# Kernel optimization log

Hardware: AMD Instinct MI355X
Metric: run time of the kernel (lower is better)

## Reference

```python
import jax, jax.numpy as jnp
import numpy as np

D = 1024   # input_size == hidden_size (tied weights)
H = 1024
V = 32000
STEPS = 5  # mogrify_steps
B = 32
T = 64


def _mogrify(x, h, W, b):
    # W: [STEPS, H, H] (square since D == H), b: [STEPS, H]
    for i in range(STEPS):
        if (i + 1) % 2 == 0:
            h = 2.0 * jax.nn.sigmoid(x @ W[i].T + b[i]) * h
        else:
            x = 2.0 * jax.nn.sigmoid(h @ W[i].T + b[i]) * x
    return x, h


def _lstm_cell(x, h, c, W_ih, W_hh, b_ih, b_hh):
    g = x @ W_ih.T + b_ih + h @ W_hh.T + b_hh  # [B, 4H], gate order i,f,g,o
    i, f, gg, o = jnp.split(g, 4, axis=-1)
    c = jax.nn.sigmoid(f) * c + jax.nn.sigmoid(i) * jnp.tanh(gg)
    h = jax.nn.sigmoid(o) * jnp.tanh(c)
    return h, c


def setup_inputs() -> dict:
    key = jax.random.key(0)
    ks = jax.random.split(key, 16)
    s = 1.0 / np.sqrt(H)
    u = lambda k, shape: jax.random.uniform(k, shape, jnp.float32, -s, s)
    return {
        "seq": jax.random.randint(ks[0], (B, T), 0, V),
        "max_len": T,
        "emb": jax.random.normal(ks[1], (V, D), jnp.float32) * 0.02,  # tied with fc weight
        "mog1_W": u(ks[2], (STEPS, H, H)), "mog1_b": u(ks[3], (STEPS, H)),
        "W_ih1": u(ks[4], (4 * H, D)), "W_hh1": u(ks[5], (4 * H, H)),
        "b_ih1": u(ks[6], (4 * H,)), "b_hh1": u(ks[7], (4 * H,)),
        "mog2_W": u(ks[8], (STEPS, H, H)), "mog2_b": u(ks[9], (STEPS, H)),
        "W_ih2": u(ks[10], (4 * H, H)), "W_hh2": u(ks[11], (4 * H, H)),
        "b_ih2": u(ks[12], (4 * H,)), "b_hh2": u(ks[13], (4 * H,)),
        "fc_b": u(ks[14], (V,)),
    }


def reference(seq, max_len, emb, mog1_W, mog1_b, W_ih1, W_hh1, b_ih1, b_hh1,
              mog2_W, mog2_b, W_ih2, W_hh2, b_ih2, b_hh2, fc_b):
    batch = seq.shape[0]
    embed = emb[seq[:, :max_len]]              # [B, T, D]
    xs = jnp.transpose(embed, (1, 0, 2))       # [T, B, D]
    h1 = jnp.zeros((batch, H), embed.dtype)
    c1 = jnp.zeros((batch, H), embed.dtype)
    h2 = jnp.zeros((batch, H), embed.dtype)
    c2 = jnp.zeros((batch, H), embed.dtype)

    def step(carry, x):
        h1, c1, h2, c2 = carry
        x1, h1m = _mogrify(x, h1, mog1_W, mog1_b)
        h1, c1 = _lstm_cell(x1, h1m, c1, W_ih1, W_hh1, b_ih1, b_hh1)
        x2, h2m = _mogrify(h1, h2, mog2_W, mog2_b)
        h2, c2 = _lstm_cell(x2, h2m, c2, W_ih2, W_hh2, b_ih2, b_hh2)
        return (h1, c1, h2, c2), h2

    _, hs = jax.lax.scan(step, (h1, c1, h2, c2), xs)   # hs: [T, B, H]
    hidden_states = jnp.transpose(hs, (1, 0, 2))        # [B, T, H]
    # fc weight tied to embedding -> logits = h @ emb.T + b (single big GEMM)
    outputs = jnp.einsum('bth,vh->btv', hidden_states, emb) + fc_b  # [B, T, V]
    return outputs, hidden_states
```

## Files before the change

### kernel.cpp

```cpp
#include <hip/hip_runtime.h>

typedef short bf16x8 __attribute__((ext_vector_type(8)));
typedef float f32x4 __attribute__((ext_vector_type(4)));
typedef unsigned int u32;
typedef u32 u32x4 __attribute__((ext_vector_type(4)));
typedef unsigned short u16;
typedef unsigned long long u64;

static __device__ __forceinline__ unsigned short f2bf(float f) {
    unsigned int u = __float_as_uint(f);
    unsigned int r = (u + 0x7fffu + ((u >> 16) & 1u)) >> 16;
    return (unsigned short)r;
}
static __device__ __forceinline__ float sigmoidf_(float x) {
    return 1.0f / (1.0f + __expf(-x));
}
static __device__ __forceinline__ float tanhf_(float x) {
    return 2.0f / (1.0f + __expf(-2.0f * x)) - 1.0f;
}

static __device__ __forceinline__ u32 pkhi(float a, float b) {
    return (__float_as_uint(a) >> 16) | (__float_as_uint(b) & 0xffff0000u);
}
static __device__ __forceinline__ u32 pklo(float a, float b) {
    float la = a - __uint_as_float(__float_as_uint(a) & 0xffff0000u);
    float lb = b - __uint_as_float(__float_as_uint(b) & 0xffff0000u);
    return (__float_as_uint(la) >> 16) | (__float_as_uint(lb) & 0xffff0000u);
}
static __device__ __forceinline__ bf16x8 mkfrag(u32 a, u32 b, u32 c, u32 d) {
    u32x4 v = {a, b, c, d};
    return __builtin_bit_cast(bf16x8, v);
}

static __device__ __forceinline__ bf16x8 ldA(const u16* p) {
    u64 a = __hip_atomic_load((const u64*)p, __ATOMIC_RELAXED, __HIP_MEMORY_SCOPE_AGENT);
    u64 b = __hip_atomic_load((const u64*)(p + 4), __ATOMIC_RELAXED, __HIP_MEMORY_SCOPE_AGENT);
    union { u64 q[2]; bf16x8 v; } u;
    u.q[0] = a; u.q[1] = b;
    return u.v;
}
static __device__ __forceinline__ float ldc4(const float* p) {
    return __hip_atomic_load(p, __ATOMIC_RELAXED, __HIP_MEMORY_SCOPE_AGENT);
}
static __device__ __forceinline__ void stc4(float* p, float v) {
    __hip_atomic_store(p, v, __ATOMIC_RELAXED, __HIP_MEMORY_SCOPE_AGENT);
}
static __device__ __forceinline__ void stc2(u16* p, u16 v) {
    __hip_atomic_store(p, v, __ATOMIC_RELAXED, __HIP_MEMORY_SCOPE_AGENT);
}

static __device__ __forceinline__ void dma16(const float* g, float* l) {
    __builtin_amdgcn_global_load_lds((const __attribute__((address_space(1))) void*)g,
                                     (__attribute__((address_space(3))) void*)l, 16, 0, 0);
}

static __device__ __forceinline__ void arrA(u32* bar, int line) {
    asm volatile("s_waitcnt vmcnt(0) lgkmcnt(0)" ::: "memory");
    __builtin_amdgcn_s_barrier();
    if (threadIdx.x == 0)
        __hip_atomic_fetch_add(bar + line * 32, 1u, __ATOMIC_RELAXED, __HIP_MEMORY_SCOPE_AGENT);
}
static __device__ __forceinline__ void arrP(u32* bar, int line) {
    __builtin_amdgcn_s_barrier();
    if (threadIdx.x == 0)
        __hip_atomic_fetch_add(bar + line * 32, 1u, __ATOMIC_RELAXED, __HIP_MEMORY_SCOPE_AGENT);
}
static __device__ __forceinline__ void bwait(u32* bar, int layer, bool master,
                                             bool glob, u32 target) {
    if (master) {
        if (threadIdx.x < 64) {
            const u32 tgt = glob ? (target << 8) : (target << 7);
            int line = glob ? (int)threadIdx.x : layer * 32 + (int)(threadIdx.x & 31);
            bool on = glob || (threadIdx.x < 32);
            for (;;) {
                u32 v = on ? __hip_atomic_load(bar + line * 32, __ATOMIC_RELAXED,
                                               __HIP_MEMORY_SCOPE_AGENT) : 0u;
                v += __shfl_xor(v, 1);
                v += __shfl_xor(v, 2);
                v += __shfl_xor(v, 4);
                v += __shfl_xor(v, 8);
                v += __shfl_xor(v, 16);
                v += __shfl_xor(v, 32);
                if (v >= tgt) break;
                __builtin_amdgcn_s_sleep(1);
            }
            if (threadIdx.x == 0)
                __hip_atomic_store(bar + 2112 + layer * 32, target, __ATOMIC_RELAXED,
                                   __HIP_MEMORY_SCOPE_AGENT);
        }
    } else {
        if (threadIdx.x == 0) {
            while (__hip_atomic_load(bar + 2112 + layer * 32, __ATOMIC_RELAXED,
                                     __HIP_MEMORY_SCOPE_AGENT) < target)
                __builtin_amdgcn_s_sleep(1);
        }
    }
    __builtin_amdgcn_s_barrier();
    asm volatile("" ::: "memory");
}

static __device__ __forceinline__ void stage_mogF(const float* W, int jb, float* lbuf,
                                                  int lane, int wv) {
    int oct2 = lane >> 5, row = (lane >> 1) & 15, half = lane & 1;
#pragma unroll
    for (int i = 0; i < 16; ++i) {
        int og = wv * 16 + i;
        const float* src = W + (size_t)(jb + row) * 1024 + (og * 2 + oct2) * 8 + half * 4;
        dma16(src, lbuf + og * 256);
    }
}
static __device__ __forceinline__ void stage_l128(const float* Ws, int jb, int kb,
                                                  float* lbuf, int lane, int wv) {
    int half = lane & 1;
#pragma unroll
    for (int i = 0; i < 8; ++i) {
        int octl = wv * 4 + (i >> 1);
        int rh = i & 1;
        int rowc = rh * 32 + (lane >> 1);
        int grow = (rowc >> 4) * 1024 + jb + (rowc & 15);
        const float* src = Ws + (size_t)grow * 1024 + kb + octl * 8 + half * 4;
        dma16(src, lbuf + octl * 512 + rh * 256);
    }
}

static __device__ __forceinline__ void l_acts(const u16* aH, const u16* aL, int cidx,
                                              int lane, int wv, bf16x8 fr[4]) {
    const int col = lane & 15, kq4 = lane >> 4;
    size_t octa = (size_t)cidx * 16 + wv * 4 + kq4;
    const u16* pH = aH + (octa * 32 + col) * 8;
    const u16* pL = aL + (octa * 32 + col) * 8;
    fr[0] = ldA(pH);
    fr[1] = ldA(pH + 128);
    fr[2] = ldA(pL);
    fr[3] = ldA(pL + 128);
}
static __device__ __forceinline__ void l_mfma(const float* lbuf, const bf16x8 fr[4],
                                              int lane, int wv, f32x4 (&acc)[4][2]) {
    const int col = lane & 15, kq4 = lane >> 4;
    const float* wbase = lbuf + (wv * 4 + kq4) * 512;
#pragma unroll
    for (int rt = 0; rt < 4; ++rt) {
        const float* wp = wbase + (rt * 16 + col) * 8;
        f32x4 w0 = *(const f32x4*)wp, w1 = *(const f32x4*)(wp + 4);
        bf16x8 whi = mkfrag(pkhi(w0.x, w0.y), pkhi(w0.z, w0.w),
                            pkhi(w1.x, w1.y), pkhi(w1.z, w1.w));
        bf16x8 wlo = mkfrag(pklo(w0.x, w0.y), pklo(w0.z, w0.w),
                            pklo(w1.x, w1.y), pklo(w1.z, w1.w));
        acc[rt][0] = __builtin_amdgcn_mfma_f32_16x16x32_bf16(fr[0], whi, acc[rt][0], 0, 0, 0);
        acc[rt][0] = __builtin_amdgcn_mfma_f32_16x16x32_bf16(fr[2], whi, acc[rt][0], 0, 0, 0);
        acc[rt][0] = __builtin_amdgcn_mfma_f32_16x16x32_bf16(fr[0], wlo, acc[rt][0], 0, 0, 0);
        acc[rt][1] = __builtin_amdgcn_mfma_f32_16x16x32_bf16(fr[1], whi, acc[rt][1], 0, 0, 0);
        acc[rt][1] = __builtin_amdgcn_mfma_f32_16x16x32_bf16(fr[3], whi, acc[rt][1], 0, 0, 0);
        acc[rt][1] = __builtin_amdgcn_mfma_f32_16x16x32_bf16(fr[1], wlo, acc[rt][1], 0, 0, 0);
    }
}

struct RArgs {
    const float *m1W, *m1b, *Wih1, *Whh1, *bih1, *bhh1;
    const float *m2W, *m2b, *Wih2, *Whh2, *bih2, *bhh2;
    float* XTF;
    u16 *XTH, *XTL;
    float* stF;
    u16* stH;
    float* hs;
    u32* bar;
};

__global__ __launch_bounds__(256, 1) void reck(RArgs A) {
    __shared__ float wbuf[4][8192];
    __shared__ float red[4][32][16];

    const int tid = threadIdx.x, lane = tid & 63, wv = tid >> 6;
    const int col = lane & 15, kq4 = lane >> 4;
    const int blk = blockIdx.x;
    const int layer = blk >> 7;
    const int g = blk & 127;
    const bool isMog = g < 64;
    const bool master = (g == 0);
    const int line = layer * 32 + (g & 31);
    const int jb = (g & 63) * 16;

    const float* mW  = layer ? A.m2W : A.m1W;
    const float* mb_ = layer ? A.m2b : A.m1b;
    const float* Wih = layer ? A.Wih2 : A.Wih1;
    const float* Whh = layer ? A.Whh2 : A.Whh1;
    const float* bih = layer ? A.bih2 : A.bih1;
    const float* bhh = layer ? A.bhh2 : A.bhh1;

    float* hF  = A.stF + layer * 32768;
    float* hmF = A.stF + 65536 + layer * 32768;
    float* cS  = A.stF + 131072 + layer * 32768;
    float* rFb = A.stF + 196608;
    u16* hH  = A.stH + layer * 32768;
    u16* hmH = A.stH + 65536 + layer * 32768;
    u16* rHb = A.stH + 131072;
    u16* hL  = A.stH + 196608 + layer * 32768;
    u16* hmL = A.stH + 262144 + layer * 32768;
    u16* rLb = A.stH + 327680;

    float* mbuf0 = &wbuf[0][0];
    float* mbuf1 = &wbuf[2][0];

    u32 bcnt = 0;
    int cur = 0;

    if (isMog) stage_mogF(mW, jb, mbuf0, lane, wv);

    for (int s = 0; s <= 64; ++s) {
        const bool act = layer ? (s > 0) : (s < 64);
        const int t = layer ? s - 1 : s;
        const int tt = act ? t : 0;
        const int rb = tt & 1;

        float* xF; u16 *xH, *xL;
        if (layer == 0) {
            xF = A.XTF + (size_t)tt * 32768;
            xH = A.XTH + (size_t)tt * 32768;
            xL = A.XTL + (size_t)tt * 32768;
        } else {
            xF = rFb + rb * 32768;
            xH = rHb + rb * 32768;
            xL = rLb + rb * 32768;
        }

        if (isMog) {
            for (int ph = 0; ph < 5; ++ph) {
                float* wsrc = cur ? mbuf1 : mbuf0;
                float* wdst = cur ? mbuf0 : mbuf1;
                if (act) {
                    const u16 *gH, *gL; const float* srcF; float* dF; u16 *dH, *dL;
                    switch (ph) {
                        case 0:  gH = hH;  gL = hL;  srcF = xF;  dF = xF;  dH = xH;  dL = xL;  break;
                        case 1:  gH = xH;  gL = xL;  srcF = hF;  dF = hmF; dH = hmH; dL = hmL; break;
                        case 2:  gH = hmH; gL = hmL; srcF = xF;  dF = xF;  dH = xH;  dL = xL;  break;
                        case 3:  gH = xH;  gL = xL;  srcF = hmF; dF = hmF; dH = hmH; dL = hmL; break;
                        default: gH = hmH; gL = hmL; srcF = xF;  dF = xF;  dH = xH;  dL = xL;  break;
                    }
                    bf16x8 AH0[8], AH1[8], AL0[8], AL1[8];
#pragma unroll
                    for (int kt = 0; kt < 8; ++kt) {
                        int octc = wv * 32 + kt * 4 + kq4;
                        const u16* pH = gH + ((size_t)octc * 32 + col) * 8;
                        const u16* pL = gL + ((size_t)octc * 32 + col) * 8;
                        AH0[kt] = ldA(pH);  AH1[kt] = ldA(pH + 128);
                        AL0[kt] = ldA(pL);  AL1[kt] = ldA(pL + 128);
                    }
                    stage_mogF(mW + (size_t)((ph + 1) % 5) * 1048576, jb, wdst, lane, wv);
                    f32x4 a0 = {0.f, 0.f, 0.f, 0.f}, a1 = {0.f, 0.f, 0.f, 0.f};
#pragma unroll
                    for (int kt = 0; kt < 8; ++kt) {
                        int octc = wv * 32 + kt * 4 + kq4;
                        const float* wp = wsrc + octc * 128 + col * 8;
                        f32x4 w0 = *(const f32x4*)wp, w1 = *(const f32x4*)(wp + 4);
                        bf16x8 whi = mkfrag(pkhi(w0.x, w0.y), pkhi(w0.z, w0.w),
                                            pkhi(w1.x, w1.y), pkhi(w1.z, w1.w));
                        bf16x8 wlo = mkfrag(pklo(w0.x, w0.y), pklo(w0.z, w0.w),
                                            pklo(w1.x, w1.y), pklo(w1.z, w1.w));
                        a0 = __builtin_amdgcn_mfma_f32_16x16x32_bf16(AH0[kt], whi, a0, 0, 0, 0);
                        a0 = __builtin_amdgcn_mfma_f32_16x16x32_bf16(AL0[kt], whi, a0, 0, 0, 0);
                        a0 = __builtin_amdgcn_mfma_f32_16x16x32_bf16(AH0[kt], wlo, a0, 0, 0, 0);
                        a1 = __builtin_amdgcn_mfma_f32_16x16x32_bf16(AH1[kt], whi, a1, 0, 0, 0);
                        a1 = __builtin_amdgcn_mfma_f32_16x16x32_bf16(AL1[kt], whi, a1, 0, 0, 0);
                        a1 = __builtin_amdgcn_mfma_f32_16x16x32_bf16(AH1[kt], wlo, a1, 0, 0, 0);
                    }
#pragma unroll
                    for (int mh = 0; mh < 2; ++mh) {
                        f32x4 av = mh ? a1 : a0;
#pragma unroll
                        for (int r = 0; r < 4; ++r)
                            red[wv][mh * 16 + kq4 * 4 + r][col] = av[r];
                    }
                    __syncthreads();
#pragma unroll
                    for (int uu = 0; uu < 2; ++uu) {
                        int u = tid + uu * 256;
                        int jj = u & 15, bb = u >> 4;
                        float sv = red[0][bb][jj] + red[1][bb][jj]
                                 + red[2][bb][jj] + red[3][bb][jj];
                        int d = jb + jj;
                        sv += mb_[ph * 1024 + d];
                        float gate = 2.0f * sigmoidf_(sv);
                        size_t pidx = ((size_t)(d >> 3) * 32 + bb) * 8 + (d & 7);
                        float val = gate * ldc4(srcF + pidx);
                        stc4(dF + pidx, val);
                        u32 uv = __float_as_uint(val);
                        stc2(dH + pidx, (u16)(uv >> 16));
                        float lov = val - __uint_as_float(uv & 0xffff0000u);
                        stc2(dL + pidx, (u16)(__float_as_uint(lov) >> 16));
                    }
                } else {
                    stage_mogF(mW + (size_t)((ph + 1) % 5) * 1048576, jb, wdst, lane, wv);
                }
                arrA(A.bar, line);
                ++bcnt;
                bwait(A.bar, layer, master, false, bcnt);
                cur ^= 1;
            }
            arrP(A.bar, line);
            ++bcnt;
            bwait(A.bar, layer, master, true, bcnt);
        } else {
            if (act) {
#pragma unroll
                for (int c = 0; c < 4; ++c)
                    stage_l128(Whh, jb, c * 128, &wbuf[c][0], lane, wv);
            }
#pragma unroll
            for (int p = 0; p < 4; ++p) {
                arrP(A.bar, line);
                ++bcnt;
                bwait(A.bar, layer, false, false, bcnt);
            }
            arrP(A.bar, line);
            ++bcnt;
            u32 g5t = bcnt;
            f32x4 acc[4][2];
#pragma unroll
            for (int rt = 0; rt < 4; ++rt) {
                acc[rt][0] = (f32x4){0.f, 0.f, 0.f, 0.f};
                acc[rt][1] = (f32x4){0.f, 0.f, 0.f, 0.f};
            }
            if (act) {
                for (int c = 0; c < 8; ++c) {
                    bf16x8 fr[4];
                    l_acts(hmH, hmL, c, lane, wv, fr);
                    l_mfma(&wbuf[c & 3][0], fr, lane, wv, acc);
                    int cn = c + 4;
                    if (cn < 8) stage_l128(Whh, jb, cn * 128, &wbuf[cn & 3][0], lane, wv);
                    else        stage_l128(Wih, jb, (cn - 8) * 128, &wbuf[cn & 3][0], lane, wv);
                }
            }
            bwait(A.bar, layer, false, false, g5t);
            if (act) {
                for (int c = 8; c < 16; ++c) {
                    bf16x8 fr[4];
                    l_acts(xH, xL, c - 8, lane, wv, fr);
                    l_mfma(&wbuf[c & 3][0], fr, lane, wv, acc);
                    int cn = c + 4;
                    if (cn < 16) stage_l128(Wih, jb, (cn - 8) * 128, &wbuf[cn & 3][0], lane, wv);
                }
                float gv[2][4];
#pragma unroll
                for (int gt = 0; gt < 4; ++gt) {
                    __syncthreads();
#pragma unroll
                    for (int mh = 0; mh < 2; ++mh) {
                        f32x4 av = acc[gt][mh];
#pragma unroll
                        for (int r = 0; r < 4; ++r)
                            red[wv][mh * 16 + kq4 * 4 + r][col] = av[r];
                    }
                    __syncthreads();
#pragma unroll
                    for (int uu = 0; uu < 2; ++uu) {
                        int u = tid + uu * 256;
                        gv[uu][gt] = red[0][u >> 4][u & 15] + red[1][u >> 4][u & 15]
                                   + red[2][u >> 4][u & 15] + red[3][u >> 4][u & 15];
                    }
                }
#pragma unroll
                for (int uu = 0; uu < 2; ++uu) {
                    int u = tid + uu * 256;
                    int cell = u & 15, bb = u >> 4;
                    int d = jb + cell;
                    float gi = gv[uu][0] + bih[d] + bhh[d];
                    float gf = gv[uu][1] + bih[1024 + d] + bhh[1024 + d];
                    float gg = gv[uu][2] + bih[2048 + d] + bhh[2048 + d];
                    float go = gv[uu][3] + bih[3072 + d] + bhh[3072 + d];
                    int cidx = d * 32 + bb;
                    float cn = sigmoidf_(gf) * cS[cidx] + sigmoidf_(gi) * tanhf_(gg);
                    cS[cidx] = cn;
                    float hn = sigmoidf_(go) * tanhf_(cn);
                    size_t pidx = ((size_t)(d >> 3) * 32 + bb) * 8 + (d & 7);
                    u32 uv = __float_as_uint(hn);
                    u16 hhi = (u16)(uv >> 16);
                    float lov = hn - __uint_as_float(uv & 0xffff0000u);
                    u16 hlo = (u16)(__float_as_uint(lov) >> 16);
                    stc4(hF + pidx, hn);
                    stc2(hH + pidx, hhi);
                    stc2(hL + pidx, hlo);
                    if (layer == 0) {
                        int wb = s & 1;
                        stc4(rFb + wb * 32768 + pidx, hn);
                        stc2(rHb + wb * 32768 + pidx, hhi);
                        stc2(rLb + wb * 32768 + pidx, hlo);
                    } else {
                        A.hs[(size_t)bb * 65536 + (size_t)t * 1024 + d] = hn;
                    }
                }
                arrA(A.bar, line);
            } else {
                arrP(A.bar, line);
            }
            ++bcnt;
            bwait(A.bar, layer, false, true, bcnt);
        }
    }
}

__global__ __launch_bounds__(256) void gather_embed(const int* __restrict__ seq,
                                                    const float* __restrict__ emb,
                                                    float* __restrict__ XTF,
                                                    u16* __restrict__ XTH,
                                                    u16* __restrict__ XTL) {
    int t = blockIdx.x;
#pragma unroll 4
    for (int i = 0; i < 16; ++i) {
        int u = i * 256 + threadIdx.x;
        int oct = u >> 5, b = u & 31;
        int row = seq[b * 64 + t];
        const float* sp = emb + (size_t)row * 1024 + oct * 8;
        float4 f0 = *(const float4*)sp;
        float4 f1 = *(const float4*)(sp + 4);
        size_t base = (size_t)t * 32768 + ((size_t)oct * 32 + b) * 8;
        *(float4*)(XTF + base) = f0;
        *(float4*)(XTF + base + 4) = f1;
        u32x4 hi = {pkhi(f0.x, f0.y), pkhi(f0.z, f0.w), pkhi(f1.x, f1.y), pkhi(f1.z, f1.w)};
        u32x4 lo = {pklo(f0.x, f0.y), pklo(f0.z, f0.w), pklo(f1.x, f1.y), pklo(f1.z, f1.w)};
        *(u32x4*)(XTH + base) = hi;
        *(u32x4*)(XTL + base) = lo;
    }
}

__global__ __launch_bounds__(256) void f32_to_bf16(const float* __restrict__ in,
                                                   unsigned short* __restrict__ out, int n) {
    int i = (blockIdx.x * 256 + threadIdx.x) * 8;
    if (i + 7 < n) {
        float4 f0 = *(const float4*)(in + i);
        float4 f1 = *(const float4*)(in + i + 4);
        bf16x8 v;
        v[0] = (short)f2bf(f0.x); v[1] = (short)f2bf(f0.y);
        v[2] = (short)f2bf(f0.z); v[3] = (short)f2bf(f0.w);
        v[4] = (short)f2bf(f1.x); v[5] = (short)f2bf(f1.y);
        v[6] = (short)f2bf(f1.z); v[7] = (short)f2bf(f1.w);
        *(bf16x8*)(out + i) = v;
    }
}

__global__ __launch_bounds__(256) void out_proj(const unsigned short* __restrict__ hsb,
                                                const float* __restrict__ emb,
                                                const float* __restrict__ fcb,
                                                float* __restrict__ out) {
    __shared__ unsigned short Al[128 * 40];
    __shared__ unsigned short Bl[128 * 40];
    int tid = threadIdx.x;
    int n0 = blockIdx.x * 128;
    int m0 = blockIdx.y * 128;
    int wid = tid >> 6, l = tid & 63;
    int wm = wid >> 1, wn = wid & 1;
    int c16 = l & 15, kg = l >> 4;

    f32x4 acc[4][4];
#pragma unroll
    for (int i = 0; i < 4; i++)
#pragma unroll
        for (int j = 0; j < 4; j++) acc[i][j] = (f32x4){0.f, 0.f, 0.f, 0.f};

    for (int k0 = 0; k0 < 1024; k0 += 32) {
#pragma unroll
        for (int i = 0; i < 2; i++) {
            int id = i * 256 + tid;
            int r = id >> 2, ccc = id & 3;
            *(bf16x8*)&Al[r * 40 + ccc * 8] =
                *(const bf16x8*)(hsb + (size_t)(m0 + r) * 1024 + k0 + ccc * 8);
        }
#pragma unroll
        for (int i = 0; i < 2; i++) {
            int id = i * 256 + tid;
            int r = id >> 2, ccc = id & 3;
            const float* src = emb + (size_t)(n0 + r) * 1024 + k0 + ccc * 8;
            float4 f0 = *(const float4*)(src);
            float4 f1 = *(const float4*)(src + 4);
            bf16x8 v;
            v[0] = (short)f2bf(f0.x); v[1] = (short)f2bf(f0.y);
            v[2] = (short)f2bf(f0.z); v[3] = (short)f2bf(f0.w);
            v[4] = (short)f2bf(f1.x); v[5] = (short)f2bf(f1.y);
            v[6] = (short)f2bf(f1.z); v[7] = (short)f2bf(f1.w);
            *(bf16x8*)&Bl[r * 40 + ccc * 8] = v;
        }
        __syncthreads();

        bf16x8 afr[4], bfr[4];
#pragma unroll
        for (int i = 0; i < 4; i++)
            afr[i] = *(const bf16x8*)&Al[(wm * 64 + i * 16 + c16) * 40 + kg * 8];
#pragma unroll
        for (int j = 0; j < 4; j++)
            bfr[j] = *(const bf16x8*)&Bl[(wn * 64 + j * 16 + c16) * 40 + kg * 8];
#pragma unroll
        for (int i = 0; i < 4; i++)
#pragma unroll
            for (int j = 0; j < 4; j++)
                acc[i][j] = __builtin_amdgcn_mfma_f32_16x16x32_bf16(afr[i], bfr[j], acc[i][j], 0, 0, 0);
        __syncthreads();
    }

#pragma unroll
    for (int i = 0; i < 4; i++) {
        int row = m0 + wm * 64 + i * 16 + kg * 4;
#pragma unroll
        for (int j = 0; j < 4; j++) {
            int col = n0 + wn * 64 + j * 16 + c16;
            float fb = fcb[col];
#pragma unroll
            for (int r = 0; r < 4; r++)
                out[(size_t)(row + r) * 32000 + col] = acc[i][j][r] + fb;
        }
    }
}

extern "C" void kernel_launch(void* const* d_in, const int* in_sizes, int n_in,
                              void* d_out, int out_size, void* d_ws, size_t ws_size,
                              hipStream_t stream) {
    const int*   seq    = (const int*)d_in[0];
    const float* emb    = (const float*)d_in[2];
    const float* mog1_W = (const float*)d_in[3];
    const float* mog1_b = (const float*)d_in[4];
    const float* W_ih1  = (const float*)d_in[5];
    const float* W_hh1  = (const float*)d_in[6];
    const float* b_ih1  = (const float*)d_in[7];
    const float* b_hh1  = (const float*)d_in[8];
    const float* mog2_W = (const float*)d_in[9];
    const float* mog2_b = (const float*)d_in[10];
    const float* W_ih2  = (const float*)d_in[11];
    const float* W_hh2  = (const float*)d_in[12];
    const float* b_ih2  = (const float*)d_in[13];
    const float* b_hh2  = (const float*)d_in[14];
    const float* fc_b   = (const float*)d_in[15];

    char* ws = (char*)d_ws;
    float* XTF = (float*)ws;
    u16*   XTH = (u16*)(ws + 8388608);
    u16*   XTL = (u16*)(ws + 12582912);
    float* stF = (float*)(ws + 16777216);
    u16*   stH = (u16*)(ws + 17825792);
    u32*   bar = (u32*)(ws + 18874368);
    unsigned short* hsb = (unsigned short*)(ws + 18890752);

    float* out0 = (float*)d_out;
    float* hs   = out0 + 65536000LL;

    hipMemsetAsync(stF, 0, 1835008, stream);
    hipMemsetAsync(bar, 0, 16384, stream);

    gather_embed<<<64, 256, 0, stream>>>(seq, emb, XTF, XTH, XTL);

    RArgs a;
    a.m1W = mog1_W; a.m1b = mog1_b;
    a.Wih1 = W_ih1; a.Whh1 = W_hh1; a.bih1 = b_ih1; a.bhh1 = b_hh1;
    a.m2W = mog2_W; a.m2b = mog2_b;
    a.Wih2 = W_ih2; a.Whh2 = W_hh2; a.bih2 = b_ih2; a.bhh2 = b_hh2;
    a.XTF = XTF; a.XTH = XTH; a.XTL = XTL;
    a.stF = stF; a.stH = stH; a.hs = hs; a.bar = bar;

    reck<<<256, 256, 0, stream>>>(a);

    f32_to_bf16<<<1024, 256, 0, stream>>>(hs, hsb, 2097152);
    out_proj<<<dim3(250, 16), 256, 0, stream>>>(hsb, emb, fc_b, out0);
}
```

Baseline: 3.968 ms.

## Decentralize grid barrier polling and prefetch weights across barrier waits

After: 4.222 ms. 6.4% more time.

```diff
diff --git a/kernel.cpp b/kernel.cpp
--- a/kernel.cpp
+++ b/kernel.cpp
@@ -54,7 +54,7 @@
                                      (__attribute__((address_space(3))) void*)l, 16, 0, 0);
 }
 
-static __device__ __forceinline__ void arrA(u32* bar, int line) {
+static __device__ __forceinline__ void arrD(u32* bar, int line) {
     asm volatile("s_waitcnt vmcnt(0) lgkmcnt(0)" ::: "memory");
     __builtin_amdgcn_s_barrier();
     if (threadIdx.x == 0)
@@ -65,34 +65,22 @@
     if (threadIdx.x == 0)
         __hip_atomic_fetch_add(bar + line * 32, 1u, __ATOMIC_RELAXED, __HIP_MEMORY_SCOPE_AGENT);
 }
-static __device__ __forceinline__ void bwait(u32* bar, int layer, bool master,
-                                             bool glob, u32 target) {
-    if (master) {
-        if (threadIdx.x < 64) {
-            const u32 tgt = glob ? (target << 8) : (target << 7);
-            int line = glob ? (int)threadIdx.x : layer * 32 + (int)(threadIdx.x & 31);
-            bool on = glob || (threadIdx.x < 32);
-            for (;;) {
-                u32 v = on ? __hip_atomic_load(bar + line * 32, __ATOMIC_RELAXED,
-                                               __HIP_MEMORY_SCOPE_AGENT) : 0u;
-                v += __shfl_xor(v, 1);
-                v += __shfl_xor(v, 2);
-                v += __shfl_xor(v, 4);
-                v += __shfl_xor(v, 8);
-                v += __shfl_xor(v, 16);
-                v += __shfl_xor(v, 32);
-                if (v >= tgt) break;
-                __builtin_amdgcn_s_sleep(1);
-            }
-            if (threadIdx.x == 0)
-                __hip_atomic_store(bar + 2112 + layer * 32, target, __ATOMIC_RELAXED,
-                                   __HIP_MEMORY_SCOPE_AGENT);
-        }
-    } else {
-        if (threadIdx.x == 0) {
-            while (__hip_atomic_load(bar + 2112 + layer * 32, __ATOMIC_RELAXED,
-                                     __HIP_MEMORY_SCOPE_AGENT) < target)
-                __builtin_amdgcn_s_sleep(1);
+static __device__ __forceinline__ void bwaitSD(u32* bar, int layer, bool glob, u32 target) {
+    if (threadIdx.x < 64) {
+        const bool on = glob || (threadIdx.x < 32);
+        const int line = glob ? (int)threadIdx.x : layer * 32 + (int)(threadIdx.x & 31);
+        const u32 tgt = glob ? (target << 8) : (target << 7);
+        for (;;) {
+            u32 v = on ? __hip_atomic_load(bar + line * 32, __ATOMIC_RELAXED,
+                                           __HIP_MEMORY_SCOPE_AGENT) : 0u;
+            v += __shfl_xor(v, 1);
+            v += __shfl_xor(v, 2);
+            v += __shfl_xor(v, 4);
+            v += __shfl_xor(v, 8);
+            v += __shfl_xor(v, 16);
+            v += __shfl_xor(v, 32);
+            if (v >= tgt) break;
+            __builtin_amdgcn_s_sleep(1);
         }
     }
     __builtin_amdgcn_s_barrier();
@@ -176,7 +164,6 @@
     const int layer = blk >> 7;
     const int g = blk & 127;
     const bool isMog = g < 64;
-    const bool master = (g == 0);
     const int line = layer * 32 + (g & 31);
     const int jb = (g & 63) * 16;
 
@@ -245,7 +232,7 @@
                         AH0[kt] = ldA(pH);  AH1[kt] = ldA(pH + 128);
                         AL0[kt] = ldA(pL);  AL1[kt] = ldA(pL + 128);
                     }
-                    stage_mogF(mW + (size_t)((ph + 1) % 5) * 1048576, jb, wdst, lane, wv);
+                    asm volatile("s_waitcnt vmcnt(63)" ::: "memory");
                     f32x4 a0 = {0.f, 0.f, 0.f, 0.f}, a1 = {0.f, 0.f, 0.f, 0.f};
 #pragma unroll
                     for (int kt = 0; kt < 8; ++kt) {
@@ -288,28 +275,31 @@
                         float lov = val - __uint_as_float(uv & 0xffff0000u);
                         stc2(dL + pidx, (u16)(__float_as_uint(lov) >> 16));
                     }
+                    arrD(A.bar, line);
                 } else {
-                    stage_mogF(mW + (size_t)((ph + 1) % 5) * 1048576, jb, wdst, lane, wv);
+                    arrP(A.bar, line);
                 }
-                arrA(A.bar, line);
                 ++bcnt;
-                bwait(A.bar, layer, master, false, bcnt);
+                stage_mogF(mW + (size_t)((ph + 1) % 5) * 1048576, jb, wdst, lane, wv);
+                bwaitSD(A.bar, layer, false, bcnt);
                 cur ^= 1;
             }
             arrP(A.bar, line);
             ++bcnt;
-            bwait(A.bar, layer, master, true, bcnt);
+            bwaitSD(A.bar, layer, true, bcnt);
         } else {
-            if (act) {
-#pragma unroll
-                for (int c = 0; c < 4; ++c)
+            const bool firstAct = act && (layer ? (s == 1) : (s == 0));
+            const bool nextAct = layer ? (s < 64) : (s < 63);
+            if (firstAct) {
+#pragma unroll
+                for (int c = 0; c < 3; ++c)
                     stage_l128(Whh, jb, c * 128, &wbuf[c][0], lane, wv);
             }
 #pragma unroll
             for (int p = 0; p < 4; ++p) {
                 arrP(A.bar, line);
                 ++bcnt;
-                bwait(A.bar, layer, false, false, bcnt);
+                bwaitSD(A.bar, layer, false, bcnt);
             }
             arrP(A.bar, line);
             ++bcnt;
@@ -320,24 +310,37 @@
                 acc[rt][0] = (f32x4){0.f, 0.f, 0.f, 0.f};
                 acc[rt][1] = (f32x4){0.f, 0.f, 0.f, 0.f};
             }
+            bf16x8 frA[4], frB[4];
             if (act) {
+                l_acts(hmH, hmL, 0, lane, wv, frA);
+#pragma unroll
                 for (int c = 0; c < 8; ++c) {
-                    bf16x8 fr[4];
-                    l_acts(hmH, hmL, c, lane, wv, fr);
-                    l_mfma(&wbuf[c & 3][0], fr, lane, wv, acc);
-                    int cn = c + 4;
+                    if (c < 7) {
+                        if (c & 1) l_acts(hmH, hmL, c + 1, lane, wv, frA);
+                        else       l_acts(hmH, hmL, c + 1, lane, wv, frB);
+                    }
+                    asm volatile("s_waitcnt vmcnt(32)" ::: "memory");
+                    int cn = c + 3;
                     if (cn < 8) stage_l128(Whh, jb, cn * 128, &wbuf[cn & 3][0], lane, wv);
                     else        stage_l128(Wih, jb, (cn - 8) * 128, &wbuf[cn & 3][0], lane, wv);
+                    if (c & 1) l_mfma(&wbuf[c & 3][0], frB, lane, wv, acc);
+                    else       l_mfma(&wbuf[c & 3][0], frA, lane, wv, acc);
                 }
             }
-            bwait(A.bar, layer, false, false, g5t);
+            bwaitSD(A.bar, layer, false, g5t);
             if (act) {
-                for (int c = 8; c < 16; ++c) {
-                    bf16x8 fr[4];
-                    l_acts(xH, xL, c - 8, lane, wv, fr);
-                    l_mfma(&wbuf[c & 3][0], fr, lane, wv, acc);
-                    int cn = c + 4;
-                    if (cn < 16) stage_l128(Wih, jb, (cn - 8) * 128, &wbuf[cn & 3][0], lane, wv);
+                l_acts(xH, xL, 0, lane, wv, frA);
+#pragma unroll
+                for (int c = 0; c < 8; ++c) {
+                    if (c < 7) {
+                        if (c & 1) l_acts(xH, xL, c + 1, lane, wv, frA);
+                        else       l_acts(xH, xL, c + 1, lane, wv, frB);
+                    }
+                    asm volatile("s_waitcnt vmcnt(32)" ::: "memory");
+                    int cn = c + 3;
+                    if (cn < 8) stage_l128(Wih, jb, cn * 128, &wbuf[cn & 3][0], lane, wv);
+                    if (c & 1) l_mfma(&wbuf[c & 3][0], frB, lane, wv, acc);
+                    else       l_mfma(&wbuf[c & 3][0], frA, lane, wv, acc);
                 }
                 float gv[2][4];
 #pragma unroll
@@ -388,12 +391,18 @@
                         A.hs[(size_t)bb * 65536 + (size_t)t * 1024 + d] = hn;
                     }
                 }
-                arrA(A.bar, line);
+                arrD(A.bar, line);
+                ++bcnt;
+                if (nextAct) {
+#pragma unroll
+                    for (int c = 0; c < 3; ++c)
+                        stage_l128(Whh, jb, c * 128, &wbuf[c][0], lane, wv);
+                }
             } else {
                 arrP(A.bar, line);
+                ++bcnt;
             }
-            ++bcnt;
-            bwait(A.bar, layer, false, true, bcnt);
+            bwaitSD(A.bar, layer, true, bcnt);
         }
     }
 }
@@ -540,8 +549,8 @@
     float* out0 = (float*)d_out;
     float* hs   = out0 + 65536000LL;
 
-    hipMemsetAsync(stF, 0, 1835008, stream);
-    hipMemsetAsync(bar, 0, 16384, stream);
+    (void)hipMemsetAsync(stF, 0, 1835008, stream);
+    (void)hipMemsetAsync(bar, 0, 16384, stream);
 
     gather_embed<<<64, 256, 0, stream>>>(seq, emb, XTF, XTH, XTL);
 
```
